# Kernel optimization log

Measured on AMD Instinct MI355X. Metric: run time of the kernel, lower is better.

Reference implementation:

```python
import jax, jax.numpy as jnp
import numpy as np

C = 256
BN_EPS = 1e-5


def conv1x1(x, w, b):
    # x: (B, Cin, H, W), w: (Cout, Cin), b: (Cout,)
    return jnp.einsum('bchw,oc->bohw', x, w) + b[None, :, None, None]


def setup_inputs() -> dict:
    key = jax.random.key(0)
    ks = jax.random.split(key, 12)
    B, H, W = 8, 64, 64
    s = 1.0 / np.sqrt(C)
    inp = {
        'xi': jax.random.normal(ks[0], (B, C, H, W), jnp.float32),
        'xj': jax.random.normal(ks[1], (B, C, H, W), jnp.float32),
        'g_w': jax.random.normal(ks[2], (C, C), jnp.float32) * s,
        'g_b': jax.random.normal(ks[3], (C,), jnp.float32) * s,
        'theta_w': jax.random.normal(ks[4], (C, C), jnp.float32) * s,
        'theta_b': jax.random.normal(ks[5], (C,), jnp.float32) * s,
        'phi_w': jax.random.normal(ks[6], (C, C), jnp.float32) * s,
        'phi_b': jax.random.normal(ks[7], (C,), jnp.float32) * s,
        'W_w': jax.random.normal(ks[8], (C, C), jnp.float32) * s,
        'W_b': jax.random.normal(ks[9], (C,), jnp.float32) * s,
        'bn_gamma': jnp.ones((C,), jnp.float32),
        'bn_beta': jnp.zeros((C,), jnp.float32),
    }
    return inp


def reference(xi, xj, g_w, g_b, theta_w, theta_b, phi_w, phi_b, W_w, W_b, bn_gamma, bn_beta):
    B, Cc, H, W = xi.shape
    N = H * W
    # 1x1 conv projections, flattened to token sequences
    g_x = conv1x1(xj, g_w, g_b).reshape(B, Cc, N)        # (B, C, N)
    theta_x = conv1x1(xi, theta_w, theta_b).reshape(B, Cc, N)  # (B, C, N)
    phi_x = conv1x1(xj, phi_w, phi_b).reshape(B, Cc, N)  # (B, C, N)
    # f = theta^T @ phi, scaled by N (no softmax)
    f = jnp.einsum('bcn,bcm->bnm', theta_x, phi_x) / N   # (B, N, N)
    # y = f @ g^T, back to channel-first
    y = jnp.einsum('bnm,bcm->bcn', f, g_x).reshape(B, Cc, H, W)
    W_y = conv1x1(y, W_w, W_b)
    z = W_y + xi
    # BatchNorm2d (training-mode batch statistics, biased variance)
    mean = jnp.mean(z, axis=(0, 2, 3), keepdims=True)
    var = jnp.var(z, axis=(0, 2, 3), keepdims=True)
    z_hat = (z - mean) * jax.lax.rsqrt(var + BN_EPS)
    return z_hat * bn_gamma[None, :, None, None] + bn_beta[None, :, None, None]
```

## Files before the change

kernel.cpp:

```cpp
#include <hip/hip_runtime.h>
#include <cstddef>

#define CCH 256
#define NPIX 4096
#define NB 8
#define INVCNT (1.0f/32768.0f)
#define INVN (1.0f/4096.0f)

typedef __bf16 bf16_t;
typedef __attribute__((ext_vector_type(8))) __bf16 bf16x8;
typedef __attribute__((ext_vector_type(4))) __bf16 bf16x4;
typedef __attribute__((ext_vector_type(4))) float f32x4;

#define OFF_S      0u
#define OFF_AB     2048u
#define OFF_BMT    34816u
#define OFF_T1     67584u
#define OFF_R      67840u
#define OFF_W1     68096u
#define OFF_C1     68352u
#define OFF_G      68608u
#define OFF_MP     592896u
#define OFF_E      855040u
#define OFF_RSP    857088u
#define OFF_ZPS    889856u
#define OFF_ZPQ    1020928u
#define OFF_SCALE  1152000u
#define OFF_SHIFT  1152256u
#define OFF_GP     1152512u
#define OFF_XIT    7443968u

__device__ __forceinline__ void pack8(const float4& x, const float4& y, bf16x8& o) {
  o[0]=(bf16_t)x.x; o[1]=(bf16_t)x.y; o[2]=(bf16_t)x.z; o[3]=(bf16_t)x.w;
  o[4]=(bf16_t)y.x; o[5]=(bf16_t)y.y; o[6]=(bf16_t)y.z; o[7]=(bf16_t)y.w;
}

__device__ __forceinline__ void ld4(const float* p, float4& a0, float4& a1, float4& a2, float4& a3) {
  a0 = *(const float4*)p;       a1 = *(const float4*)(p + 4);
  a2 = *(const float4*)(p + 8); a3 = *(const float4*)(p + 12);
}

template <bool ATRANS>
__device__ __forceinline__ void mm64_compute(const float* __restrict__ A,
                                             const float* __restrict__ B,
                                             int i0, int j0,
                                             float (&acc)[4][4],
                                             float (*s1)[65], float (*s2)[65]) {
  const int t = threadIdx.x, tx = t & 15, ty = t >> 4;
  for (int k0 = 0; k0 < 256; k0 += 64) {
#pragma unroll
    for (int it = 0; it < 4; ++it) {
      const int f = t + 256 * it;
      const int row = f >> 4, cc = (f & 15) * 4;
      float4 va;
      if (ATRANS)
        va = *(const float4*)(A + (size_t)(k0 + row) * CCH + i0 + cc);
      else
        va = *(const float4*)(A + (size_t)(i0 + row) * CCH + k0 + cc);
      const float4 vb = *(const float4*)(B + (size_t)(k0 + row) * CCH + j0 + cc);
      s1[row][cc + 0] = va.x; s1[row][cc + 1] = va.y; s1[row][cc + 2] = va.z; s1[row][cc + 3] = va.w;
      s2[row][cc + 0] = vb.x; s2[row][cc + 1] = vb.y; s2[row][cc + 2] = vb.z; s2[row][cc + 3] = vb.w;
    }
    __syncthreads();
#pragma unroll 4
    for (int kk = 0; kk < 64; ++kk) {
      float ar[4], br[4];
#pragma unroll
      for (int i = 0; i < 4; ++i) ar[i] = ATRANS ? s1[kk][4 * ty + i] : s1[4 * ty + i][kk];
#pragma unroll
      for (int j = 0; j < 4; ++j) br[j] = s2[kk][4 * tx + j];
#pragma unroll
      for (int i = 0; i < 4; ++i)
#pragma unroll
        for (int j = 0; j < 4; ++j) acc[i][j] += ar[i] * br[j];
    }
    __syncthreads();
  }
}

__device__ void pre_body(int blk, const float* Ww, const float* gw, const float* phw,
                         const float* thw, const float* gb, const float* phb,
                         const float* thb, float* ws, unsigned char* SMEM) {
  const int t = threadIdx.x;
  if (blk < 32) {
    float (*s1)[65] = (float(*)[65])SMEM;
    float (*s2)[65] = (float(*)[65])(SMEM + 16640);
    const int tb = blk & 15;
    const int i0 = (tb >> 2) * 64, j0 = (tb & 3) * 64;
    float acc[4][4] = {};
    if (blk < 16) mm64_compute<false>(Ww, gw, i0, j0, acc, s1, s2);
    else          mm64_compute<true >(thw, phw, i0, j0, acc, s1, s2);
    bf16_t* outp = (bf16_t*)(ws + (blk < 16 ? OFF_AB : OFF_BMT));
    const int tx = t & 15, ty = t >> 4;
#pragma unroll
    for (int i = 0; i < 4; ++i) {
      bf16x4 mv;
#pragma unroll
      for (int q = 0; q < 4; ++q) mv[q] = (bf16_t)acc[i][q];
      *(bf16x4*)&outp[(size_t)(i0 + 4 * ty + i) * CCH + j0 + 4 * tx] = mv;
    }
  } else {
    float t1v = 0.f, rv = 0.f, w1v = 0.f;
    for (int k = 0; k < 256; ++k) {
      t1v += phw[k * CCH + t] * thb[k];
      rv  += thw[k * CCH + t] * phb[k];
      w1v += Ww[t * CCH + k] * gb[k];
    }
    ws[OFF_T1 + t] = t1v; ws[OFF_R + t] = rv; ws[OFF_W1 + t] = w1v;
    float* red = (float*)SMEM;
    red[t] = phb[t] * thb[t];
    __syncthreads();
    for (int off = 128; off; off >>= 1) { if (t < off) red[t] += red[t + off]; __syncthreads(); }
    if (t == 0) ws[OFF_C1] = red[0];
  }
}

__device__ void cvtT_body(int bx, int b, const float* __restrict__ xi,
                          float* __restrict__ ws, unsigned char* SMEM) {
  bf16_t (*st)[72] = (bf16_t(*)[72])SMEM;
  const int c0 = (bx & 3) * 64;
  const int n0 = (bx >> 2) * 64;
  const float* X = xi + (size_t)b * CCH * NPIX;
  const int t = threadIdx.x;
  const int r = t >> 4, c4 = (t & 15) * 4;
#pragma unroll
  for (int it = 0; it < 4; ++it) {
    const int row = r + 16 * it;
    const float4 v = *(const float4*)(X + (size_t)(c0 + row) * NPIX + n0 + c4);
    st[row][c4 + 0] = (bf16_t)v.x; st[row][c4 + 1] = (bf16_t)v.y;
    st[row][c4 + 2] = (bf16_t)v.z; st[row][c4 + 3] = (bf16_t)v.w;
  }
  __syncthreads();
  bf16_t* Xit = (bf16_t*)(ws + OFF_XIT) + (size_t)b * NPIX * CCH;
  const int nr = t >> 2, cc = (t & 3) * 16;
  bf16x8 o0, o1;
#pragma unroll
  for (int j = 0; j < 8; ++j) o0[j] = st[cc + j][nr];
#pragma unroll
  for (int j = 0; j < 8; ++j) o1[j] = st[cc + 8 + j][nr];
  *(bf16x8*)(Xit + (size_t)(n0 + nr) * CCH + c0 + cc) = o0;
  *(bf16x8*)(Xit + (size_t)(n0 + nr) * CCH + c0 + cc + 8) = o1;
}

__device__ void gram_body(int bx, int b, const float* __restrict__ xj,
                          float* __restrict__ ws, unsigned char* SMEM) {
  const int ks = bx & 15;
  const int tl = bx >> 4;
  const int i0 = (tl == 2) ? 128 : 0;
  const int j0 = (tl == 0) ? 0 : 128;
  const float* __restrict__ X = xj + (size_t)b * CCH * NPIX;
  bf16_t (*sA)[128][40] = (bf16_t(*)[128][40])SMEM;
  bf16_t (*sB)[128][40] = (bf16_t(*)[128][40])(SMEM + 20480);
  const int t = threadIdx.x;
  const int w = t >> 6, lane = t & 63;
  const f32x4 z4 = {0.f, 0.f, 0.f, 0.f};
  f32x4 acc[2][8];
#pragma unroll
  for (int fr = 0; fr < 2; ++fr)
#pragma unroll
    for (int fc = 0; fc < 8; ++fc) acc[fr][fc] = z4;
  float rsum = 0.f;
  const int k0 = ks * 256;
  const int srow = t >> 1, sh16 = (t & 1) * 16;
  const bool haveB = (tl == 1);

  float4 a0, a1, a2, a3, b0, b1, b2, b3;
  auto LOAD = [&](int kc) {
    const float* pa = X + (size_t)(i0 + srow) * NPIX + k0 + kc + sh16;
    ld4(pa, a0, a1, a2, a3);
    rsum += a0.x + a0.y + a0.z + a0.w + a1.x + a1.y + a1.z + a1.w
          + a2.x + a2.y + a2.z + a2.w + a3.x + a3.y + a3.z + a3.w;
    if (haveB) {
      const float* pb = X + (size_t)(j0 + srow) * NPIX + k0 + kc + sh16;
      ld4(pb, b0, b1, b2, b3);
    }
  };
  auto WRITE = [&](int q) {
    bf16x8 u0, u1;
    pack8(a0, a1, u0); pack8(a2, a3, u1);
    *(bf16x8*)&sA[q][srow][sh16] = u0;
    *(bf16x8*)&sA[q][srow][sh16 + 8] = u1;
    if (haveB) {
      bf16x8 w0, w1;
      pack8(b0, b1, w0); pack8(b2, b3, w1);
      *(bf16x8*)&sB[q][srow][sh16] = w0;
      *(bf16x8*)&sB[q][srow][sh16 + 8] = w1;
    }
  };

  LOAD(0);
  WRITE(0);
  __syncthreads();
  int cur = 0;
  for (int kc8 = 0; kc8 < 8; ++kc8) {
    if (kc8 < 7) LOAD(32 * (kc8 + 1));
    const int fcol = 8 * (lane >> 4);
    const int lr = lane & 15;
    bf16_t (*SBc)[40] = haveB ? sB[cur] : sA[cur];
    const bf16x8 af0 = *(const bf16x8*)&sA[cur][32 * w + lr][fcol];
    const bf16x8 af1 = *(const bf16x8*)&sA[cur][32 * w + 16 + lr][fcol];
#pragma unroll
    for (int fc = 0; fc < 8; ++fc) {
      const bf16x8 bv = *(const bf16x8*)&SBc[16 * fc + lr][fcol];
      acc[0][fc] = __builtin_amdgcn_mfma_f32_16x16x32_bf16(af0, bv, acc[0][fc], 0, 0, 0);
      acc[1][fc] = __builtin_amdgcn_mfma_f32_16x16x32_bf16(af1, bv, acc[1][fc], 0, 0, 0);
    }
    if (kc8 < 7) WRITE(cur ^ 1);
    __syncthreads();
    cur ^= 1;
  }

  if (tl != 1) {
    const float o = __shfl_down(rsum, 1);
    if (!(t & 1)) ws[OFF_RSP + ((size_t)(b * 16 + ks)) * CCH + i0 + srow] = rsum + o;
  }
  float* GP = ws + OFF_GP + ((size_t)((b * 16 + ks) * 3 + tl)) * 16384;
  const int rbase = 32 * w + ((lane >> 4) << 2);
  const int col = lane & 15;
#pragma unroll
  for (int fr = 0; fr < 2; ++fr)
#pragma unroll
    for (int fc = 0; fc < 8; ++fc)
#pragma unroll
      for (int reg = 0; reg < 4; ++reg)
        GP[(size_t)(rbase + 16 * fr + reg) * 128 + 16 * fc + col] = acc[fr][fc][reg];
}

__global__ __launch_bounds__(256) void k_mega(const float* __restrict__ xi,
                                              const float* __restrict__ xj,
                                              const float* __restrict__ Ww,
                                              const float* __restrict__ gw,
                                              const float* __restrict__ phw,
                                              const float* __restrict__ thw,
                                              const float* __restrict__ gb,
                                              const float* __restrict__ phb,
                                              const float* __restrict__ thb,
                                              float* __restrict__ ws) {
  __shared__ __align__(16) unsigned char SMEM[40960];
  const int bx = blockIdx.x, by = blockIdx.y;
  if (bx >= 304) {
    if (by == 0) pre_body(bx - 304, Ww, gw, phw, thw, gb, phb, thb, ws, SMEM);
    return;
  }
  if (bx >= 48) { cvtT_body(bx - 48, by, xi, ws, SMEM); return; }
  gram_body(bx, by, xj, ws, SMEM);
}

__global__ __launch_bounds__(256) void k_greduce(float* __restrict__ ws) {
  const int b = blockIdx.y, bx = blockIdx.x, t = threadIdx.x;
  const float* BP = ws + OFF_GP + (size_t)b * 48 * 16384;
  float* G = ws + OFF_G + (size_t)b * 65536;
  if (bx < 128) {
    const int i = bx;
    const int j = t;
    const int tl = (j < 128) ? 0 : 1;
    const size_t idx = (size_t)i * 128 + (j & 127);
    float s = 0.f;
#pragma unroll 4
    for (int ks = 0; ks < 16; ++ks) s += BP[((size_t)ks * 3 + tl) * 16384 + idx];
    G[(size_t)i * CCH + j] = s;
    if (j >= 128) G[(size_t)j * CCH + i] = s;
    if (t < 32) {
      const int row = (t < 16) ? i : (i + 128);
      const int l = t & 15;
      float v = ws[OFF_RSP + ((size_t)(b * 16 + l)) * CCH + row];
#pragma unroll
      for (int off = 8; off; off >>= 1) v += __shfl_down(v, off, 16);
      if (l == 0) ws[OFF_S + b * CCH + row] = v;
    }
  } else {
    const int r = 128 + ((bx - 128) << 1) + (t >> 7);
    const int j = 128 + (t & 127);
    const size_t idx = (size_t)(r - 128) * 128 + (j - 128);
    float s = 0.f;
#pragma unroll 4
    for (int ks = 0; ks < 16; ++ks) s += BP[((size_t)ks * 3 + 2) * 16384 + idx];
    G[(size_t)r * CCH + j] = s;
  }
}

__global__ __launch_bounds__(256) void k_kmmat(const float* __restrict__ Wb, float* __restrict__ ws) {
  const int b = blockIdx.y;
  const int i0 = blockIdx.x * 64;
  const int t = threadIdx.x;
  const int w = t >> 6, lane = t & 63;
  const int rg = w >> 1, cg = w & 1;
  const int lr = lane & 15, hi = lane >> 4;
  const int fcol = 8 * hi;

  __shared__ __align__(16) bf16_t sA[2][64][40];
  __shared__ __align__(16) bf16_t sB[2][256][40];
  __shared__ __align__(16) bf16_t sK[64][264];
  __shared__ float sS[256], sT1[256], sR[256], sW1[256], sVS[256];
  __shared__ float sU[64];
  __shared__ float red[256];
  __shared__ float sdt_sh;

  const bf16_t* Ab  = (const bf16_t*)(ws + OFF_AB);
  const bf16_t* BmT = (const bf16_t*)(ws + OFF_BMT);
  const float*  Gf  = ws + OFF_G + (size_t)b * 65536;

  sS[t]  = ws[OFF_S + b * CCH + t];
  sT1[t] = ws[OFF_T1 + t];
  sR[t]  = ws[OFF_R + t];
  sW1[t] = ws[OFF_W1 + t];
  __syncthreads();
  red[t] = sS[t] * sT1[t];
  __syncthreads();
  for (int off = 128; off; off >>= 1) { if (t < off) red[t] += red[t + off]; __syncthreads(); }
  if (t == 0) sdt_sh = red[0];
  {
    float a = 0.f;
    for (int k8 = 0; k8 < 256; k8 += 8) {
      const bf16x8 v = *(const bf16x8*)&BmT[(size_t)t * CCH + k8];
#pragma unroll
      for (int q = 0; q < 8; ++q) a += (float)v[q] * sS[k8 + q];
    }
    sVS[t] = a;
  }
  if (t < 64) {
    float a = 0.f;
    for (int k8 = 0; k8 < 256; k8 += 8) {
      const bf16x8 v = *(const bf16x8*)&Ab[(size_t)(i0 + t) * CCH + k8];
#pragma unroll
      for (int q = 0; q < 8; ++q) a += (float)v[q] * sS[k8 + q];
    }
    sU[t] = a;
  }

  const f32x4 z4 = {0.f, 0.f, 0.f, 0.f};
  const int arow = t >> 2, achk = (t & 3) * 8;

  f32x4 acc[2][8];
#pragma unroll
  for (int fr = 0; fr < 2; ++fr)
#pragma unroll
    for (int fc = 0; fc < 8; ++fc) acc[fr][fc] = z4;
  bf16x8 ra;
  float4 g[4][2];
  auto LOADB = [&](int k) {
    ra = *(const bf16x8*)&Ab[(size_t)(i0 + arow) * CCH + k + achk];
#pragma unroll
    for (int h = 0; h < 4; ++h) {
      const float* p = &Gf[(size_t)(64 * h + arow) * CCH + k + achk];
      g[h][0] = *(const float4*)p;
      g[h][1] = *(const float4*)(p + 4);
    }
  };
  auto WRITEB = [&](int q) {
    *(bf16x8*)&sA[q][arow][achk] = ra;
#pragma unroll
    for (int h = 0; h < 4; ++h) {
      bf16x8 u;
      pack8(g[h][0], g[h][1], u);
      *(bf16x8*)&sB[q][64 * h + arow][achk] = u;
    }
  };
  LOADB(0);
  WRITEB(0);
  __syncthreads();
  int cur = 0;
  for (int ks = 0; ks < 8; ++ks) {
    if (ks < 7) LOADB(32 * (ks + 1));
    const bf16x8 af0 = *(const bf16x8*)&sA[cur][32 * rg + lr][fcol];
    const bf16x8 af1 = *(const bf16x8*)&sA[cur][32 * rg + 16 + lr][fcol];
#pragma unroll
    for (int fc = 0; fc < 8; ++fc) {
      const bf16x8 bv = *(const bf16x8*)&sB[cur][128 * cg + 16 * fc + lr][fcol];
      acc[0][fc] = __builtin_amdgcn_mfma_f32_16x16x32_bf16(af0, bv, acc[0][fc], 0, 0, 0);
      acc[1][fc] = __builtin_amdgcn_mfma_f32_16x16x32_bf16(af1, bv, acc[1][fc], 0, 0, 0);
    }
    if (ks < 7) WRITEB(cur ^ 1);
    __syncthreads();
    cur ^= 1;
  }
#pragma unroll
  for (int fr = 0; fr < 2; ++fr)
#pragma unroll
    for (int fc = 0; fc < 8; ++fc)
#pragma unroll
      for (int reg = 0; reg < 4; ++reg)
        sK[32 * rg + 16 * fr + 4 * hi + reg][128 * cg + 16 * fc + lr] = (bf16_t)acc[fr][fc][reg];
  __syncthreads();

  if (t < 64) {
    float dot = 0.f;
    for (int k8 = 0; k8 < 256; k8 += 8) {
      const bf16x8 v = *(const bf16x8*)&sK[t][k8];
#pragma unroll
      for (int q = 0; q < 8; ++q) dot += (float)v[q] * sT1[k8 + q];
    }
    const float c1 = ws[OFF_C1];
    const float ui = sU[t], w1i = sW1[i0 + t];
    ws[OFF_E + b * CCH + i0 + t] = INVN * (dot + c1 * ui + sdt_sh * w1i) + c1 * w1i + Wb[i0 + t];
  }

  f32x4 acc2[2][8];
#pragma unroll
  for (int fr = 0; fr < 2; ++fr)
#pragma unroll
    for (int fc = 0; fc < 8; ++fc) acc2[fr][fc] = z4;
  bf16x8 rb[4];
  auto LOADC = [&](int k) {
#pragma unroll
    for (int h = 0; h < 4; ++h)
      rb[h] = *(const bf16x8*)&BmT[(size_t)(64 * h + arow) * CCH + k + achk];
  };
  auto WRITEC = [&](int q) {
#pragma unroll
    for (int h = 0; h < 4; ++h)
      *(bf16x8*)&sB[q][64 * h + arow][achk] = rb[h];
  };
  LOADC(0);
  WRITEC(0);
  __syncthreads();
  cur = 0;
  for (int ks = 0; ks < 8; ++ks) {
    if (ks < 7) LOADC(32 * (ks + 1));
    const bf16x8 af0 = *(const bf16x8*)&sK[32 * rg + lr][32 * ks + fcol];
    const bf16x8 af1 = *(const bf16x8*)&sK[32 * rg + 16 + lr][32 * ks + fcol];
#pragma unroll
    for (int fc = 0; fc < 8; ++fc) {
      const bf16x8 bv = *(const bf16x8*)&sB[cur][128 * cg + 16 * fc + lr][fcol];
      acc2[0][fc] = __builtin_amdgcn_mfma_f32_16x16x32_bf16(af0, bv, acc2[0][fc], 0, 0, 0);
      acc2[1][fc] = __builtin_amdgcn_mfma_f32_16x16x32_bf16(af1, bv, acc2[1][fc], 0, 0, 0);
    }
    if (ks < 7) WRITEC(cur ^ 1);
    __syncthreads();
    cur ^= 1;
  }

  bf16_t* Mp = (bf16_t*)(ws + OFF_MP) + (size_t)b * 65536;
#pragma unroll
  for (int fr = 0; fr < 2; ++fr)
#pragma unroll
    for (int fc = 0; fc < 8; ++fc) {
      const int j = 128 * cg + 16 * fc + lr;
      const float rj = sR[j], vsj = sVS[j];
#pragma unroll
      for (int reg = 0; reg < 4; ++reg) {
        const int il = 32 * rg + 16 * fr + 4 * hi + reg;
        const float ui = sU[il], w1i = sW1[i0 + il];
        float m = (acc2[fr][fc][reg] + ui * rj + w1i * vsj) * INVN + w1i * rj;
        if (i0 + il == j) m += 1.0f;
        Mp[(size_t)(i0 + il) * CCH + j] = (bf16_t)m;
      }
    }
}

template <int APPLY>
__global__ __launch_bounds__(256) void k_zmm(float* __restrict__ ws, float* __restrict__ out) {
  const int b = blockIdx.y, nblk = blockIdx.x;
  const int n0 = nblk * 64;
  const int t = threadIdx.x;
  const int w = t >> 6, lane = t & 63;
  const int rg = w >> 1, cg = w & 1;
  __shared__ __align__(16) bf16_t sA[2][64][40];
  __shared__ __align__(16) bf16_t sB[2][256][40];
  __shared__ float sC1[256], sC2[256];
  __shared__ float redS[4][128], redQ[4][128];
  {
    const float e = ws[OFF_E + b * CCH + t];
    if (APPLY) {
      const float sc = ws[OFF_SCALE + t];
      sC1[t] = sc;
      sC2[t] = e * sc + ws[OFF_SHIFT + t];
    } else {
      sC1[t] = e;
    }
  }
  const bf16_t* Xit = (const bf16_t*)(ws + OFF_XIT) + (size_t)b * NPIX * CCH;
  const bf16_t* Mp = (const bf16_t*)(ws + OFF_MP) + (size_t)b * 65536;
  const f32x4 z4 = {0.f, 0.f, 0.f, 0.f};
  f32x4 acc[2][8];
#pragma unroll
  for (int fr = 0; fr < 2; ++fr)
#pragma unroll
    for (int fc = 0; fc < 8; ++fc) acc[fr][fc] = z4;
  const int arow = t >> 2, achk = (t & 3) * 8;
  bf16x8 ra, rb0, rb1, rb2, rb3;
  ra  = *(const bf16x8*)(Xit + (size_t)(n0 + arow) * CCH + achk);
  rb0 = *(const bf16x8*)(Mp + (size_t)(arow)       * CCH + achk);
  rb1 = *(const bf16x8*)(Mp + (size_t)(64 + arow)  * CCH + achk);
  rb2 = *(const bf16x8*)(Mp + (size_t)(128 + arow) * CCH + achk);
  rb3 = *(const bf16x8*)(Mp + (size_t)(192 + arow) * CCH + achk);
  *(bf16x8*)&sA[0][arow][achk] = ra;
  *(bf16x8*)&sB[0][arow][achk] = rb0;
  *(bf16x8*)&sB[0][64 + arow][achk] = rb1;
  *(bf16x8*)&sB[0][128 + arow][achk] = rb2;
  *(bf16x8*)&sB[0][192 + arow][achk] = rb3;
  __syncthreads();
  int cur = 0;
  for (int ks = 0; ks < 8; ++ks) {
    const int nk = 32 * (ks + 1);
    if (ks < 7) {
      ra  = *(const bf16x8*)(Xit + (size_t)(n0 + arow) * CCH + nk + achk);
      rb0 = *(const bf16x8*)(Mp + (size_t)(arow)       * CCH + nk + achk);
      rb1 = *(const bf16x8*)(Mp + (size_t)(64 + arow)  * CCH + nk + achk);
      rb2 = *(const bf16x8*)(Mp + (size_t)(128 + arow) * CCH + nk + achk);
      rb3 = *(const bf16x8*)(Mp + (size_t)(192 + arow) * CCH + nk + achk);
    }
    const int fcol = 8 * (lane >> 4);
    const int lr = lane & 15;
    const bf16x8 af0 = *(const bf16x8*)&sA[cur][32 * rg + lr][fcol];
    const bf16x8 af1 = *(const bf16x8*)&sA[cur][32 * rg + 16 + lr][fcol];
#pragma unroll
    for (int fc = 0; fc < 8; ++fc) {
      const bf16x8 bv = *(const bf16x8*)&sB[cur][128 * cg + 16 * fc + lr][fcol];
      acc[0][fc] = __builtin_amdgcn_mfma_f32_16x16x32_bf16(af0, bv, acc[0][fc], 0, 0, 0);
      acc[1][fc] = __builtin_amdgcn_mfma_f32_16x16x32_bf16(af1, bv, acc[1][fc], 0, 0, 0);
    }
    if (ks < 7) {
      *(bf16x8*)&sA[cur ^ 1][arow][achk] = ra;
      *(bf16x8*)&sB[cur ^ 1][arow][achk] = rb0;
      *(bf16x8*)&sB[cur ^ 1][64 + arow][achk] = rb1;
      *(bf16x8*)&sB[cur ^ 1][128 + arow][achk] = rb2;
      *(bf16x8*)&sB[cur ^ 1][192 + arow][achk] = rb3;
    }
    __syncthreads();
    cur ^= 1;
  }
  if (APPLY) {
#pragma unroll
    for (int fc = 0; fc < 8; ++fc) {
      const int c = 128 * cg + 16 * fc + (lane & 15);
      const float sc = sC1[c], b2 = sC2[c];
      float* op = out + ((size_t)b * CCH + c) * NPIX + n0 + 32 * rg + ((lane >> 4) << 2);
#pragma unroll
      for (int fr = 0; fr < 2; ++fr) {
        float4 v;
        v.x = acc[fr][fc][0] * sc + b2;
        v.y = acc[fr][fc][1] * sc + b2;
        v.z = acc[fr][fc][2] * sc + b2;
        v.w = acc[fr][fc][3] * sc + b2;
        *(float4*)(op + 16 * fr) = v;
      }
    }
  } else {
    float ps[8], pq[8];
#pragma unroll
    for (int fc = 0; fc < 8; ++fc) {
      const int c = 128 * cg + 16 * fc + (lane & 15);
      const float e = sC1[c];
      float s = 0.f, q = 0.f;
#pragma unroll
      for (int fr = 0; fr < 2; ++fr)
#pragma unroll
        for (int reg = 0; reg < 4; ++reg) {
          const float z = acc[fr][fc][reg] + e;
          s += z; q += z * z;
        }
      s += __shfl_xor(s, 16); s += __shfl_xor(s, 32);
      q += __shfl_xor(q, 16); q += __shfl_xor(q, 32);
      ps[fc] = s; pq[fc] = q;
    }
    if (lane < 16) {
#pragma unroll
      for (int fc = 0; fc < 8; ++fc) {
        redS[w][16 * fc + lane] = ps[fc];
        redQ[w][16 * fc + lane] = pq[fc];
      }
    }
    __syncthreads();
    if (t < 256) {
      const int cg2 = t >> 7, c = t & 127;
      float s = 0.f, q = 0.f;
#pragma unroll
      for (int rg2 = 0; rg2 < 2; ++rg2) {
        s += redS[rg2 * 2 + cg2][c];
        q += redQ[rg2 * 2 + cg2][c];
      }
      ws[OFF_ZPS + (size_t)t * 512 + b * 64 + nblk] = s;
      ws[OFF_ZPQ + (size_t)t * 512 + b * 64 + nblk] = q;
    }
  }
}

__global__ __launch_bounds__(64) void k_bnstats(const float* __restrict__ gamma,
                                                const float* __restrict__ beta,
                                                float* __restrict__ ws) {
  const int c = blockIdx.x, t = threadIdx.x;
  const float* PS = ws + OFF_ZPS + (size_t)c * 512;
  const float* PQ = ws + OFF_ZPQ + (size_t)c * 512;
  float s = 0.f, q = 0.f;
#pragma unroll
  for (int e = 0; e < 8; ++e) { s += PS[t + 64 * e]; q += PQ[t + 64 * e]; }
#pragma unroll
  for (int off = 32; off; off >>= 1) { s += __shfl_down(s, off); q += __shfl_down(q, off); }
  if (t == 0) {
    const float mean = s * INVCNT;
    const float var = q * INVCNT - mean * mean;
    const float sc = gamma[c] * rsqrtf(var + 1e-5f);
    ws[OFF_SCALE + c] = sc;
    ws[OFF_SHIFT + c] = beta[c] - mean * sc;
  }
}

extern "C" void kernel_launch(void* const* d_in, const int* in_sizes, int n_in,
                              void* d_out, int out_size, void* d_ws, size_t ws_size,
                              hipStream_t stream) {
  const float* xi  = (const float*)d_in[0];
  const float* xj  = (const float*)d_in[1];
  const float* gw  = (const float*)d_in[2];
  const float* gb  = (const float*)d_in[3];
  const float* thw = (const float*)d_in[4];
  const float* thb = (const float*)d_in[5];
  const float* phw = (const float*)d_in[6];
  const float* phb = (const float*)d_in[7];
  const float* Ww  = (const float*)d_in[8];
  const float* Wb  = (const float*)d_in[9];
  const float* gamma = (const float*)d_in[10];
  const float* beta  = (const float*)d_in[11];
  float* ws = (float*)d_ws;
  float* out = (float*)d_out;

  k_mega<<<dim3(337, 8), 256, 0, stream>>>(xi, xj, Ww, gw, phw, thw, gb, phb, thb, ws);
  k_greduce<<<dim3(192, 8), 256, 0, stream>>>(ws);
  k_kmmat<<<dim3(4, 8), 256, 0, stream>>>(Wb, ws);
  k_zmm<0><<<dim3(64, 8), 256, 0, stream>>>(ws, out);
  k_bnstats<<<256, 64, 0, stream>>>(gamma, beta, ws);
  k_zmm<1><<<dim3(64, 8), 256, 0, stream>>>(ws, out);
}
```

Measured before the change: 98.83 us.

## Cut Gram split-K partials, store Gram in bf16, stage output stores via LDS

The Gram-matrix split-K factor drops from 16 to 4 slices per batch, so each block runs a longer K loop. This shrinks the partial-sum buffer and the reduction traffic, at the cost of fewer parallel blocks. The reduced Gram matrix is now written as bf16, which halves its storage and removes the float-to-bf16 packing in the consumer kernel, with extra rounding before the MFMA. The final normalized-output write is transposed through shared memory so each thread emits contiguous float4 runs along pixels, adding two barriers per half.

Result: slower. 108.2 us (+9.4%).

```diff
diff --git a/kernel.cpp b/kernel.cpp
--- a/kernel.cpp
+++ b/kernel.cpp
@@ -20,15 +20,15 @@
 #define OFF_W1     68096u
 #define OFF_C1     68352u
 #define OFF_G      68608u
-#define OFF_MP     592896u
-#define OFF_E      855040u
-#define OFF_RSP    857088u
-#define OFF_ZPS    889856u
-#define OFF_ZPQ    1020928u
-#define OFF_SCALE  1152000u
-#define OFF_SHIFT  1152256u
-#define OFF_GP     1152512u
-#define OFF_XIT    7443968u
+#define OFF_MP     330752u
+#define OFF_E      592896u
+#define OFF_RSP    594944u
+#define OFF_ZPS    603136u
+#define OFF_ZPQ    734208u
+#define OFF_SCALE  865280u
+#define OFF_SHIFT  865536u
+#define OFF_GP     865792u
+#define OFF_XIT    2438656u
 
 __device__ __forceinline__ void pack8(const float4& x, const float4& y, bf16x8& o) {
   o[0]=(bf16_t)x.x; o[1]=(bf16_t)x.y; o[2]=(bf16_t)x.z; o[3]=(bf16_t)x.w;
@@ -144,8 +144,8 @@
 
 __device__ void gram_body(int bx, int b, const float* __restrict__ xj,
                           float* __restrict__ ws, unsigned char* SMEM) {
-  const int ks = bx & 15;
-  const int tl = bx >> 4;
+  const int ks = bx & 3;
+  const int tl = bx >> 2;
   const int i0 = (tl == 2) ? 128 : 0;
   const int j0 = (tl == 0) ? 0 : 128;
   const float* __restrict__ X = xj + (size_t)b * CCH * NPIX;
@@ -160,7 +160,7 @@
 #pragma unroll
     for (int fc = 0; fc < 8; ++fc) acc[fr][fc] = z4;
   float rsum = 0.f;
-  const int k0 = ks * 256;
+  const int k0 = ks * 1024;
   const int srow = t >> 1, sh16 = (t & 1) * 16;
   const bool haveB = (tl == 1);
 
@@ -192,8 +192,8 @@
   WRITE(0);
   __syncthreads();
   int cur = 0;
-  for (int kc8 = 0; kc8 < 8; ++kc8) {
-    if (kc8 < 7) LOAD(32 * (kc8 + 1));
+  for (int kc8 = 0; kc8 < 32; ++kc8) {
+    if (kc8 < 31) LOAD(32 * (kc8 + 1));
     const int fcol = 8 * (lane >> 4);
     const int lr = lane & 15;
     bf16_t (*SBc)[40] = haveB ? sB[cur] : sA[cur];
@@ -205,16 +205,16 @@
       acc[0][fc] = __builtin_amdgcn_mfma_f32_16x16x32_bf16(af0, bv, acc[0][fc], 0, 0, 0);
       acc[1][fc] = __builtin_amdgcn_mfma_f32_16x16x32_bf16(af1, bv, acc[1][fc], 0, 0, 0);
     }
-    if (kc8 < 7) WRITE(cur ^ 1);
+    if (kc8 < 31) WRITE(cur ^ 1);
     __syncthreads();
     cur ^= 1;
   }
 
   if (tl != 1) {
     const float o = __shfl_down(rsum, 1);
-    if (!(t & 1)) ws[OFF_RSP + ((size_t)(b * 16 + ks)) * CCH + i0 + srow] = rsum + o;
-  }
-  float* GP = ws + OFF_GP + ((size_t)((b * 16 + ks) * 3 + tl)) * 16384;
+    if (!(t & 1)) ws[OFF_RSP + ((size_t)(b * 4 + ks)) * CCH + i0 + srow] = rsum + o;
+  }
+  float* GP = ws + OFF_GP + ((size_t)((b * 4 + ks) * 3 + tl)) * 16384;
   const int rbase = 32 * w + ((lane >> 4) << 2);
   const int col = lane & 15;
 #pragma unroll
@@ -238,32 +238,32 @@
                                               float* __restrict__ ws) {
   __shared__ __align__(16) unsigned char SMEM[40960];
   const int bx = blockIdx.x, by = blockIdx.y;
-  if (bx >= 304) {
-    if (by == 0) pre_body(bx - 304, Ww, gw, phw, thw, gb, phb, thb, ws, SMEM);
+  if (bx >= 268) {
+    if (by == 0) pre_body(bx - 268, Ww, gw, phw, thw, gb, phb, thb, ws, SMEM);
     return;
   }
-  if (bx >= 48) { cvtT_body(bx - 48, by, xi, ws, SMEM); return; }
+  if (bx >= 12) { cvtT_body(bx - 12, by, xi, ws, SMEM); return; }
   gram_body(bx, by, xj, ws, SMEM);
 }
 
 __global__ __launch_bounds__(256) void k_greduce(float* __restrict__ ws) {
   const int b = blockIdx.y, bx = blockIdx.x, t = threadIdx.x;
-  const float* BP = ws + OFF_GP + (size_t)b * 48 * 16384;
-  float* G = ws + OFF_G + (size_t)b * 65536;
+  const float* BP = ws + OFF_GP + (size_t)b * 12 * 16384;
+  bf16_t* Gb = (bf16_t*)(ws + OFF_G) + (size_t)b * 65536;
   if (bx < 128) {
     const int i = bx;
     const int j = t;
     const int tl = (j < 128) ? 0 : 1;
     const size_t idx = (size_t)i * 128 + (j & 127);
     float s = 0.f;
-#pragma unroll 4
-    for (int ks = 0; ks < 16; ++ks) s += BP[((size_t)ks * 3 + tl) * 16384 + idx];
-    G[(size_t)i * CCH + j] = s;
-    if (j >= 128) G[(size_t)j * CCH + i] = s;
+#pragma unroll
+    for (int ks = 0; ks < 4; ++ks) s += BP[((size_t)ks * 3 + tl) * 16384 + idx];
+    Gb[(size_t)i * CCH + j] = (bf16_t)s;
+    if (j >= 128) Gb[(size_t)j * CCH + i] = (bf16_t)s;
     if (t < 32) {
       const int row = (t < 16) ? i : (i + 128);
       const int l = t & 15;
-      float v = ws[OFF_RSP + ((size_t)(b * 16 + l)) * CCH + row];
+      float v = (l < 4) ? ws[OFF_RSP + ((size_t)(b * 4 + l)) * CCH + row] : 0.f;
 #pragma unroll
       for (int off = 8; off; off >>= 1) v += __shfl_down(v, off, 16);
       if (l == 0) ws[OFF_S + b * CCH + row] = v;
@@ -273,9 +273,9 @@
     const int j = 128 + (t & 127);
     const size_t idx = (size_t)(r - 128) * 128 + (j - 128);
     float s = 0.f;
-#pragma unroll 4
-    for (int ks = 0; ks < 16; ++ks) s += BP[((size_t)ks * 3 + 2) * 16384 + idx];
-    G[(size_t)r * CCH + j] = s;
+#pragma unroll
+    for (int ks = 0; ks < 4; ++ks) s += BP[((size_t)ks * 3 + 2) * 16384 + idx];
+    Gb[(size_t)r * CCH + j] = (bf16_t)s;
   }
 }
 
@@ -298,7 +298,7 @@
 
   const bf16_t* Ab  = (const bf16_t*)(ws + OFF_AB);
   const bf16_t* BmT = (const bf16_t*)(ws + OFF_BMT);
-  const float*  Gf  = ws + OFF_G + (size_t)b * 65536;
+  const bf16_t* Gb  = (const bf16_t*)(ws + OFF_G) + (size_t)b * 65536;
 
   sS[t]  = ws[OFF_S + b * CCH + t];
   sT1[t] = ws[OFF_T1 + t];
@@ -337,24 +337,18 @@
 #pragma unroll
     for (int fc = 0; fc < 8; ++fc) acc[fr][fc] = z4;
   bf16x8 ra;
-  float4 g[4][2];
+  bf16x8 gb8[4];
   auto LOADB = [&](int k) {
     ra = *(const bf16x8*)&Ab[(size_t)(i0 + arow) * CCH + k + achk];
 #pragma unroll
-    for (int h = 0; h < 4; ++h) {
-      const float* p = &Gf[(size_t)(64 * h + arow) * CCH + k + achk];
-      g[h][0] = *(const float4*)p;
-      g[h][1] = *(const float4*)(p + 4);
-    }
+    for (int h = 0; h < 4; ++h)
+      gb8[h] = *(const bf16x8*)&Gb[(size_t)(64 * h + arow) * CCH + k + achk];
   };
   auto WRITEB = [&](int q) {
     *(bf16x8*)&sA[q][arow][achk] = ra;
 #pragma unroll
-    for (int h = 0; h < 4; ++h) {
-      bf16x8 u;
-      pack8(g[h][0], g[h][1], u);
-      *(bf16x8*)&sB[q][64 * h + arow][achk] = u;
-    }
+    for (int h = 0; h < 4; ++h)
+      *(bf16x8*)&sB[q][64 * h + arow][achk] = gb8[h];
   };
   LOADB(0);
   WRITEB(0);
@@ -455,8 +449,10 @@
   const int t = threadIdx.x;
   const int w = t >> 6, lane = t & 63;
   const int rg = w >> 1, cg = w & 1;
-  __shared__ __align__(16) bf16_t sA[2][64][40];
-  __shared__ __align__(16) bf16_t sB[2][256][40];
+  __shared__ __align__(16) unsigned char SMEMu[51200];
+  bf16_t (*sA)[64][40]  = (bf16_t(*)[64][40])SMEMu;
+  bf16_t (*sB)[256][40] = (bf16_t(*)[256][40])(SMEMu + 10240);
+  float (*sZ)[68]       = (float(*)[68])SMEMu;
   __shared__ float sC1[256], sC2[256];
   __shared__ float redS[4][128], redQ[4][128];
   {
@@ -521,19 +517,31 @@
     cur ^= 1;
   }
   if (APPLY) {
-#pragma unroll
-    for (int fc = 0; fc < 8; ++fc) {
-      const int c = 128 * cg + 16 * fc + (lane & 15);
+    const int lr = lane & 15, hi = lane >> 4;
+    for (int h = 0; h < 2; ++h) {
+      __syncthreads();
+      if (cg == h) {
+#pragma unroll
+        for (int fr = 0; fr < 2; ++fr)
+#pragma unroll
+          for (int fc = 0; fc < 8; ++fc)
+#pragma unroll
+            for (int reg = 0; reg < 4; ++reg)
+              sZ[16 * fc + lr][32 * rg + 16 * fr + 4 * hi + reg] = acc[fr][fc][reg];
+      }
+      __syncthreads();
+      const int rr = t >> 1, nq = (t & 1) * 32;
+      const int c = 128 * h + rr;
       const float sc = sC1[c], b2 = sC2[c];
-      float* op = out + ((size_t)b * CCH + c) * NPIX + n0 + 32 * rg + ((lane >> 4) << 2);
-#pragma unroll
-      for (int fr = 0; fr < 2; ++fr) {
+      float* op = out + ((size_t)b * CCH + c) * NPIX + n0 + nq;
+#pragma unroll
+      for (int q = 0; q < 8; ++q) {
         float4 v;
-        v.x = acc[fr][fc][0] * sc + b2;
-        v.y = acc[fr][fc][1] * sc + b2;
-        v.z = acc[fr][fc][2] * sc + b2;
-        v.w = acc[fr][fc][3] * sc + b2;
-        *(float4*)(op + 16 * fr) = v;
+        v.x = sZ[rr][nq + 4 * q + 0] * sc + b2;
+        v.y = sZ[rr][nq + 4 * q + 1] * sc + b2;
+        v.z = sZ[rr][nq + 4 * q + 2] * sc + b2;
+        v.w = sZ[rr][nq + 4 * q + 3] * sc + b2;
+        *(float4*)(op + 4 * q) = v;
       }
     }
   } else {
@@ -614,7 +622,7 @@
   float* ws = (float*)d_ws;
   float* out = (float*)d_out;
 
-  k_mega<<<dim3(337, 8), 256, 0, stream>>>(xi, xj, Ww, gw, phw, thw, gb, phb, thb, ws);
+  k_mega<<<dim3(301, 8), 256, 0, stream>>>(xi, xj, Ww, gw, phw, thw, gb, phb, thb, ws);
   k_greduce<<<dim3(192, 8), 256, 0, stream>>>(ws);
   k_kmmat<<<dim3(4, 8), 256, 0, stream>>>(Wb, ws);
   k_zmm<0><<<dim3(64, 8), 256, 0, stream>>>(ws, out);
```

## Compute full Gram tile per block with 512 threads and store partials in bf16

Applied to the files above, without the earlier changes.

The Gram stage now has each 512-thread block compute the full 256x256 Gram partial for its K slice from one shared tile, instead of three symmetric 128x128 tiles that reloaded xj rows. Partials and the reduced G matrix are stored as bf16, which halves traffic through greduce and kmmat and lets kmmat skip the fp32-to-bf16 packing. The pre and transpose bodies are re-tiled for 512 threads, and kmmat uses 32-row tiles to double its grid. In exchange, G is now summed and stored in bf16, which loses precision, and the larger blocks with more accumulators raise register pressure.

New measurement: 87.46 us. -11.5%, faster.

```diff
diff --git a/kernel.cpp b/kernel.cpp
--- a/kernel.cpp
+++ b/kernel.cpp
@@ -20,15 +20,15 @@
 #define OFF_W1     68096u
 #define OFF_C1     68352u
 #define OFF_G      68608u
-#define OFF_MP     592896u
-#define OFF_E      855040u
-#define OFF_RSP    857088u
-#define OFF_ZPS    889856u
-#define OFF_ZPQ    1020928u
-#define OFF_SCALE  1152000u
-#define OFF_SHIFT  1152256u
-#define OFF_GP     1152512u
-#define OFF_XIT    7443968u
+#define OFF_MP     330752u
+#define OFF_E      592896u
+#define OFF_RSP    594944u
+#define OFF_ZPS    627712u
+#define OFF_ZPQ    758784u
+#define OFF_SCALE  889856u
+#define OFF_SHIFT  890112u
+#define OFF_GP     890368u
+#define OFF_XIT    5084672u
 
 __device__ __forceinline__ void pack8(const float4& x, const float4& y, bf16x8& o) {
   o[0]=(bf16_t)x.x; o[1]=(bf16_t)x.y; o[2]=(bf16_t)x.z; o[3]=(bf16_t)x.w;
@@ -41,16 +41,16 @@
 }
 
 template <bool ATRANS>
-__device__ __forceinline__ void mm64_compute(const float* __restrict__ A,
-                                             const float* __restrict__ B,
-                                             int i0, int j0,
-                                             float (&acc)[4][4],
-                                             float (*s1)[65], float (*s2)[65]) {
+__device__ __forceinline__ void mm64v(const float* __restrict__ A,
+                                      const float* __restrict__ B,
+                                      int i0, int j0,
+                                      float (&acc)[2][4],
+                                      float (*s1)[65], float (*s2)[65]) {
   const int t = threadIdx.x, tx = t & 15, ty = t >> 4;
   for (int k0 = 0; k0 < 256; k0 += 64) {
 #pragma unroll
-    for (int it = 0; it < 4; ++it) {
-      const int f = t + 256 * it;
+    for (int it = 0; it < 2; ++it) {
+      const int f = t + 512 * it;
       const int row = f >> 4, cc = (f & 15) * 4;
       float4 va;
       if (ATRANS)
@@ -64,13 +64,13 @@
     __syncthreads();
 #pragma unroll 4
     for (int kk = 0; kk < 64; ++kk) {
-      float ar[4], br[4];
-#pragma unroll
-      for (int i = 0; i < 4; ++i) ar[i] = ATRANS ? s1[kk][4 * ty + i] : s1[4 * ty + i][kk];
+      float ar[2], br[4];
+#pragma unroll
+      for (int i = 0; i < 2; ++i) ar[i] = ATRANS ? s1[kk][2 * ty + i] : s1[2 * ty + i][kk];
 #pragma unroll
       for (int j = 0; j < 4; ++j) br[j] = s2[kk][4 * tx + j];
 #pragma unroll
-      for (int i = 0; i < 4; ++i)
+      for (int i = 0; i < 2; ++i)
 #pragma unroll
         for (int j = 0; j < 4; ++j) acc[i][j] += ar[i] * br[j];
     }
@@ -87,30 +87,32 @@
     float (*s2)[65] = (float(*)[65])(SMEM + 16640);
     const int tb = blk & 15;
     const int i0 = (tb >> 2) * 64, j0 = (tb & 3) * 64;
-    float acc[4][4] = {};
-    if (blk < 16) mm64_compute<false>(Ww, gw, i0, j0, acc, s1, s2);
-    else          mm64_compute<true >(thw, phw, i0, j0, acc, s1, s2);
+    float acc[2][4] = {};
+    if (blk < 16) mm64v<false>(Ww, gw, i0, j0, acc, s1, s2);
+    else          mm64v<true >(thw, phw, i0, j0, acc, s1, s2);
     bf16_t* outp = (bf16_t*)(ws + (blk < 16 ? OFF_AB : OFF_BMT));
     const int tx = t & 15, ty = t >> 4;
 #pragma unroll
-    for (int i = 0; i < 4; ++i) {
+    for (int i = 0; i < 2; ++i) {
       bf16x4 mv;
 #pragma unroll
       for (int q = 0; q < 4; ++q) mv[q] = (bf16_t)acc[i][q];
-      *(bf16x4*)&outp[(size_t)(i0 + 4 * ty + i) * CCH + j0 + 4 * tx] = mv;
+      *(bf16x4*)&outp[(size_t)(i0 + 2 * ty + i) * CCH + j0 + 4 * tx] = mv;
     }
   } else {
-    float t1v = 0.f, rv = 0.f, w1v = 0.f;
-    for (int k = 0; k < 256; ++k) {
-      t1v += phw[k * CCH + t] * thb[k];
-      rv  += thw[k * CCH + t] * phb[k];
-      w1v += Ww[t * CCH + k] * gb[k];
-    }
-    ws[OFF_T1 + t] = t1v; ws[OFF_R + t] = rv; ws[OFF_W1 + t] = w1v;
+    if (t < 256) {
+      float t1v = 0.f, rv = 0.f, w1v = 0.f;
+      for (int k = 0; k < 256; ++k) {
+        t1v += phw[k * CCH + t] * thb[k];
+        rv  += thw[k * CCH + t] * phb[k];
+        w1v += Ww[t * CCH + k] * gb[k];
+      }
+      ws[OFF_T1 + t] = t1v; ws[OFF_R + t] = rv; ws[OFF_W1 + t] = w1v;
+    }
     float* red = (float*)SMEM;
-    red[t] = phb[t] * thb[t];
-    __syncthreads();
-    for (int off = 128; off; off >>= 1) { if (t < off) red[t] += red[t + off]; __syncthreads(); }
+    red[t] = (t < 256) ? phb[t] * thb[t] : 0.f;
+    __syncthreads();
+    for (int off = 256; off; off >>= 1) { if (t < off) red[t] += red[t + off]; __syncthreads(); }
     if (t == 0) ws[OFF_C1] = red[0];
   }
 }
@@ -118,21 +120,22 @@
 __device__ void cvtT_body(int bx, int b, const float* __restrict__ xi,
                           float* __restrict__ ws, unsigned char* SMEM) {
   bf16_t (*st)[72] = (bf16_t(*)[72])SMEM;
-  const int c0 = (bx & 3) * 64;
-  const int n0 = (bx >> 2) * 64;
+  const int c0 = (bx & 1) * 128;
+  const int n0 = (bx >> 1) * 64;
   const float* X = xi + (size_t)b * CCH * NPIX;
   const int t = threadIdx.x;
-  const int r = t >> 4, c4 = (t & 15) * 4;
-#pragma unroll
-  for (int it = 0; it < 4; ++it) {
-    const int row = r + 16 * it;
-    const float4 v = *(const float4*)(X + (size_t)(c0 + row) * NPIX + n0 + c4);
-    st[row][c4 + 0] = (bf16_t)v.x; st[row][c4 + 1] = (bf16_t)v.y;
-    st[row][c4 + 2] = (bf16_t)v.z; st[row][c4 + 3] = (bf16_t)v.w;
+  const int r = t >> 2, c4 = (t & 3) * 16;
+  {
+    float4 a0, a1, a2, a3;
+    ld4(X + (size_t)(c0 + r) * NPIX + n0 + c4, a0, a1, a2, a3);
+    bf16x8 u0, u1;
+    pack8(a0, a1, u0); pack8(a2, a3, u1);
+    *(bf16x8*)&st[r][c4] = u0;
+    *(bf16x8*)&st[r][c4 + 8] = u1;
   }
   __syncthreads();
   bf16_t* Xit = (bf16_t*)(ws + OFF_XIT) + (size_t)b * NPIX * CCH;
-  const int nr = t >> 2, cc = (t & 3) * 16;
+  const int nr = t >> 3, cc = (t & 7) * 16;
   bf16x8 o0, o1;
 #pragma unroll
   for (int j = 0; j < 8; ++j) o0[j] = st[cc + j][nr];
@@ -142,50 +145,36 @@
   *(bf16x8*)(Xit + (size_t)(n0 + nr) * CCH + c0 + cc + 8) = o1;
 }
 
-__device__ void gram_body(int bx, int b, const float* __restrict__ xj,
+__device__ void gram_body(int ks, int b, const float* __restrict__ xj,
                           float* __restrict__ ws, unsigned char* SMEM) {
-  const int ks = bx & 15;
-  const int tl = bx >> 4;
-  const int i0 = (tl == 2) ? 128 : 0;
-  const int j0 = (tl == 0) ? 0 : 128;
   const float* __restrict__ X = xj + (size_t)b * CCH * NPIX;
-  bf16_t (*sA)[128][40] = (bf16_t(*)[128][40])SMEM;
-  bf16_t (*sB)[128][40] = (bf16_t(*)[128][40])(SMEM + 20480);
+  bf16_t (*sA)[256][40] = (bf16_t(*)[256][40])SMEM;
   const int t = threadIdx.x;
   const int w = t >> 6, lane = t & 63;
+  const int wr = w >> 1, wc = w & 1;
+  const int lr = lane & 15, hi = lane >> 4;
+  const int fcol = 8 * hi;
   const f32x4 z4 = {0.f, 0.f, 0.f, 0.f};
-  f32x4 acc[2][8];
-#pragma unroll
-  for (int fr = 0; fr < 2; ++fr)
+  f32x4 acc[4][8];
+#pragma unroll
+  for (int fr = 0; fr < 4; ++fr)
 #pragma unroll
     for (int fc = 0; fc < 8; ++fc) acc[fr][fc] = z4;
   float rsum = 0.f;
   const int k0 = ks * 256;
   const int srow = t >> 1, sh16 = (t & 1) * 16;
-  const bool haveB = (tl == 1);
-
-  float4 a0, a1, a2, a3, b0, b1, b2, b3;
+
+  float4 a0, a1, a2, a3;
   auto LOAD = [&](int kc) {
-    const float* pa = X + (size_t)(i0 + srow) * NPIX + k0 + kc + sh16;
-    ld4(pa, a0, a1, a2, a3);
+    ld4(X + (size_t)srow * NPIX + k0 + kc + sh16, a0, a1, a2, a3);
     rsum += a0.x + a0.y + a0.z + a0.w + a1.x + a1.y + a1.z + a1.w
           + a2.x + a2.y + a2.z + a2.w + a3.x + a3.y + a3.z + a3.w;
-    if (haveB) {
-      const float* pb = X + (size_t)(j0 + srow) * NPIX + k0 + kc + sh16;
-      ld4(pb, b0, b1, b2, b3);
-    }
   };
   auto WRITE = [&](int q) {
     bf16x8 u0, u1;
     pack8(a0, a1, u0); pack8(a2, a3, u1);
     *(bf16x8*)&sA[q][srow][sh16] = u0;
     *(bf16x8*)&sA[q][srow][sh16 + 8] = u1;
-    if (haveB) {
-      bf16x8 w0, w1;
-      pack8(b0, b1, w0); pack8(b2, b3, w1);
-      *(bf16x8*)&sB[q][srow][sh16] = w0;
-      *(bf16x8*)&sB[q][srow][sh16 + 8] = w1;
-    }
   };
 
   LOAD(0);
@@ -194,39 +183,38 @@
   int cur = 0;
   for (int kc8 = 0; kc8 < 8; ++kc8) {
     if (kc8 < 7) LOAD(32 * (kc8 + 1));
-    const int fcol = 8 * (lane >> 4);
-    const int lr = lane & 15;
-    bf16_t (*SBc)[40] = haveB ? sB[cur] : sA[cur];
-    const bf16x8 af0 = *(const bf16x8*)&sA[cur][32 * w + lr][fcol];
-    const bf16x8 af1 = *(const bf16x8*)&sA[cur][32 * w + 16 + lr][fcol];
+    bf16x8 af[4];
+#pragma unroll
+    for (int fr = 0; fr < 4; ++fr)
+      af[fr] = *(const bf16x8*)&sA[cur][64 * wr + 16 * fr + lr][fcol];
 #pragma unroll
     for (int fc = 0; fc < 8; ++fc) {
-      const bf16x8 bv = *(const bf16x8*)&SBc[16 * fc + lr][fcol];
-      acc[0][fc] = __builtin_amdgcn_mfma_f32_16x16x32_bf16(af0, bv, acc[0][fc], 0, 0, 0);
-      acc[1][fc] = __builtin_amdgcn_mfma_f32_16x16x32_bf16(af1, bv, acc[1][fc], 0, 0, 0);
+      const bf16x8 bv = *(const bf16x8*)&sA[cur][128 * wc + 16 * fc + lr][fcol];
+#pragma unroll
+      for (int fr = 0; fr < 4; ++fr)
+        acc[fr][fc] = __builtin_amdgcn_mfma_f32_16x16x32_bf16(af[fr], bv, acc[fr][fc], 0, 0, 0);
     }
     if (kc8 < 7) WRITE(cur ^ 1);
     __syncthreads();
     cur ^= 1;
   }
 
-  if (tl != 1) {
+  {
     const float o = __shfl_down(rsum, 1);
-    if (!(t & 1)) ws[OFF_RSP + ((size_t)(b * 16 + ks)) * CCH + i0 + srow] = rsum + o;
-  }
-  float* GP = ws + OFF_GP + ((size_t)((b * 16 + ks) * 3 + tl)) * 16384;
-  const int rbase = 32 * w + ((lane >> 4) << 2);
-  const int col = lane & 15;
-#pragma unroll
-  for (int fr = 0; fr < 2; ++fr)
+    if (!(t & 1)) ws[OFF_RSP + ((size_t)(b * 16 + ks)) * CCH + srow] = rsum + o;
+  }
+  bf16_t* GPp = (bf16_t*)(ws + OFF_GP) + (size_t)(b * 16 + ks) * 65536;
+#pragma unroll
+  for (int fr = 0; fr < 4; ++fr)
 #pragma unroll
     for (int fc = 0; fc < 8; ++fc)
 #pragma unroll
       for (int reg = 0; reg < 4; ++reg)
-        GP[(size_t)(rbase + 16 * fr + reg) * 128 + 16 * fc + col] = acc[fr][fc][reg];
-}
-
-__global__ __launch_bounds__(256) void k_mega(const float* __restrict__ xi,
+        GPp[(size_t)(64 * wr + 16 * fr + 4 * hi + reg) * CCH + 128 * wc + 16 * fc + lr] =
+            (bf16_t)acc[fr][fc][reg];
+}
+
+__global__ __launch_bounds__(512) void k_mega(const float* __restrict__ xi,
                                               const float* __restrict__ xj,
                                               const float* __restrict__ Ww,
                                               const float* __restrict__ gw,
@@ -238,67 +226,60 @@
                                               float* __restrict__ ws) {
   __shared__ __align__(16) unsigned char SMEM[40960];
   const int bx = blockIdx.x, by = blockIdx.y;
-  if (bx >= 304) {
-    if (by == 0) pre_body(bx - 304, Ww, gw, phw, thw, gb, phb, thb, ws, SMEM);
+  if (bx >= 144) {
+    if (by == 0) pre_body(bx - 144, Ww, gw, phw, thw, gb, phb, thb, ws, SMEM);
     return;
   }
-  if (bx >= 48) { cvtT_body(bx - 48, by, xi, ws, SMEM); return; }
+  if (bx >= 16) { cvtT_body(bx - 16, by, xi, ws, SMEM); return; }
   gram_body(bx, by, xj, ws, SMEM);
 }
 
 __global__ __launch_bounds__(256) void k_greduce(float* __restrict__ ws) {
   const int b = blockIdx.y, bx = blockIdx.x, t = threadIdx.x;
-  const float* BP = ws + OFF_GP + (size_t)b * 48 * 16384;
-  float* G = ws + OFF_G + (size_t)b * 65536;
-  if (bx < 128) {
-    const int i = bx;
-    const int j = t;
-    const int tl = (j < 128) ? 0 : 1;
-    const size_t idx = (size_t)i * 128 + (j & 127);
-    float s = 0.f;
-#pragma unroll 4
-    for (int ks = 0; ks < 16; ++ks) s += BP[((size_t)ks * 3 + tl) * 16384 + idx];
-    G[(size_t)i * CCH + j] = s;
-    if (j >= 128) G[(size_t)j * CCH + i] = s;
-    if (t < 32) {
-      const int row = (t < 16) ? i : (i + 128);
-      const int l = t & 15;
-      float v = ws[OFF_RSP + ((size_t)(b * 16 + l)) * CCH + row];
-#pragma unroll
-      for (int off = 8; off; off >>= 1) v += __shfl_down(v, off, 16);
-      if (l == 0) ws[OFF_S + b * CCH + row] = v;
-    }
-  } else {
-    const int r = 128 + ((bx - 128) << 1) + (t >> 7);
-    const int j = 128 + (t & 127);
-    const size_t idx = (size_t)(r - 128) * 128 + (j - 128);
-    float s = 0.f;
-#pragma unroll 4
-    for (int ks = 0; ks < 16; ++ks) s += BP[((size_t)ks * 3 + 2) * 16384 + idx];
-    G[(size_t)r * CCH + j] = s;
+  const bf16_t* GPp = (const bf16_t*)(ws + OFF_GP) + (size_t)b * 16 * 65536;
+  bf16_t* Gb = (bf16_t*)(ws + OFF_G) + (size_t)b * 65536;
+  const int row = bx * 8 + (t >> 5);
+  const int j8 = (t & 31) * 8;
+  float s[8] = {};
+#pragma unroll
+  for (int ks = 0; ks < 16; ++ks) {
+    const bf16x8 v = *(const bf16x8*)&GPp[(size_t)ks * 65536 + row * CCH + j8];
+#pragma unroll
+    for (int q = 0; q < 8; ++q) s[q] += (float)v[q];
+  }
+  bf16x8 o;
+#pragma unroll
+  for (int q = 0; q < 8; ++q) o[q] = (bf16_t)s[q];
+  *(bf16x8*)&Gb[(size_t)row * CCH + j8] = o;
+  if (t < 128) {
+    const int rr = bx * 8 + (t >> 4), l = t & 15;
+    float v = ws[OFF_RSP + ((size_t)(b * 16 + l)) * CCH + rr];
+#pragma unroll
+    for (int off = 8; off; off >>= 1) v += __shfl_down(v, off, 16);
+    if (l == 0) ws[OFF_S + b * CCH + rr] = v;
   }
 }
 
 __global__ __launch_bounds__(256) void k_kmmat(const float* __restrict__ Wb, float* __restrict__ ws) {
   const int b = blockIdx.y;
-  const int i0 = blockIdx.x * 64;
+  const int i0 = blockIdx.x * 32;
   const int t = threadIdx.x;
   const int w = t >> 6, lane = t & 63;
   const int rg = w >> 1, cg = w & 1;
   const int lr = lane & 15, hi = lane >> 4;
   const int fcol = 8 * hi;
 
-  __shared__ __align__(16) bf16_t sA[2][64][40];
+  __shared__ __align__(16) bf16_t sA[2][32][40];
   __shared__ __align__(16) bf16_t sB[2][256][40];
-  __shared__ __align__(16) bf16_t sK[64][264];
+  __shared__ __align__(16) bf16_t sK[32][264];
   __shared__ float sS[256], sT1[256], sR[256], sW1[256], sVS[256];
-  __shared__ float sU[64];
+  __shared__ float sU[32];
   __shared__ float red[256];
   __shared__ float sdt_sh;
 
   const bf16_t* Ab  = (const bf16_t*)(ws + OFF_AB);
   const bf16_t* BmT = (const bf16_t*)(ws + OFF_BMT);
-  const float*  Gf  = ws + OFF_G + (size_t)b * 65536;
+  const bf16_t* Gb  = (const bf16_t*)(ws + OFF_G) + (size_t)b * 65536;
 
   sS[t]  = ws[OFF_S + b * CCH + t];
   sT1[t] = ws[OFF_T1 + t];
@@ -318,7 +299,7 @@
     }
     sVS[t] = a;
   }
-  if (t < 64) {
+  if (t < 32) {
     float a = 0.f;
     for (int k8 = 0; k8 < 256; k8 += 8) {
       const bf16x8 v = *(const bf16x8*)&Ab[(size_t)(i0 + t) * CCH + k8];
@@ -330,31 +311,24 @@
 
   const f32x4 z4 = {0.f, 0.f, 0.f, 0.f};
   const int arow = t >> 2, achk = (t & 3) * 8;
-
-  f32x4 acc[2][8];
-#pragma unroll
-  for (int fr = 0; fr < 2; ++fr)
-#pragma unroll
-    for (int fc = 0; fc < 8; ++fc) acc[fr][fc] = z4;
+  const int arA = t >> 2, akA = (t & 3) * 8;
+
+  f32x4 acc[8];
+#pragma unroll
+  for (int fc = 0; fc < 8; ++fc) acc[fc] = z4;
   bf16x8 ra;
-  float4 g[4][2];
+  bf16x8 gb8[4];
   auto LOADB = [&](int k) {
-    ra = *(const bf16x8*)&Ab[(size_t)(i0 + arow) * CCH + k + achk];
-#pragma unroll
-    for (int h = 0; h < 4; ++h) {
-      const float* p = &Gf[(size_t)(64 * h + arow) * CCH + k + achk];
-      g[h][0] = *(const float4*)p;
-      g[h][1] = *(const float4*)(p + 4);
-    }
+    if (t < 128) ra = *(const bf16x8*)&Ab[(size_t)(i0 + arA) * CCH + k + akA];
+#pragma unroll
+    for (int h = 0; h < 4; ++h)
+      gb8[h] = *(const bf16x8*)&Gb[(size_t)(64 * h + arow) * CCH + k + achk];
   };
   auto WRITEB = [&](int q) {
-    *(bf16x8*)&sA[q][arow][achk] = ra;
-#pragma unroll
-    for (int h = 0; h < 4; ++h) {
-      bf16x8 u;
-      pack8(g[h][0], g[h][1], u);
-      *(bf16x8*)&sB[q][64 * h + arow][achk] = u;
-    }
+    if (t < 128) *(bf16x8*)&sA[q][arA][akA] = ra;
+#pragma unroll
+    for (int h = 0; h < 4; ++h)
+      *(bf16x8*)&sB[q][64 * h + arow][achk] = gb8[h];
   };
   LOADB(0);
   WRITEB(0);
@@ -362,28 +336,24 @@
   int cur = 0;
   for (int ks = 0; ks < 8; ++ks) {
     if (ks < 7) LOADB(32 * (ks + 1));
-    const bf16x8 af0 = *(const bf16x8*)&sA[cur][32 * rg + lr][fcol];
-    const bf16x8 af1 = *(const bf16x8*)&sA[cur][32 * rg + 16 + lr][fcol];
+    const bf16x8 af = *(const bf16x8*)&sA[cur][16 * rg + lr][fcol];
 #pragma unroll
     for (int fc = 0; fc < 8; ++fc) {
       const bf16x8 bv = *(const bf16x8*)&sB[cur][128 * cg + 16 * fc + lr][fcol];
-      acc[0][fc] = __builtin_amdgcn_mfma_f32_16x16x32_bf16(af0, bv, acc[0][fc], 0, 0, 0);
-      acc[1][fc] = __builtin_amdgcn_mfma_f32_16x16x32_bf16(af1, bv, acc[1][fc], 0, 0, 0);
+      acc[fc] = __builtin_amdgcn_mfma_f32_16x16x32_bf16(af, bv, acc[fc], 0, 0, 0);
     }
     if (ks < 7) WRITEB(cur ^ 1);
     __syncthreads();
     cur ^= 1;
   }
 #pragma unroll
-  for (int fr = 0; fr < 2; ++fr)
-#pragma unroll
-    for (int fc = 0; fc < 8; ++fc)
-#pragma unroll
-      for (int reg = 0; reg < 4; ++reg)
-        sK[32 * rg + 16 * fr + 4 * hi + reg][128 * cg + 16 * fc + lr] = (bf16_t)acc[fr][fc][reg];
-  __syncthreads();
-
-  if (t < 64) {
+  for (int fc = 0; fc < 8; ++fc)
+#pragma unroll
+    for (int reg = 0; reg < 4; ++reg)
+      sK[16 * rg + 4 * hi + reg][128 * cg + 16 * fc + lr] = (bf16_t)acc[fc][reg];
+  __syncthreads();
+
+  if (t < 32) {
     float dot = 0.f;
     for (int k8 = 0; k8 < 256; k8 += 8) {
       const bf16x8 v = *(const bf16x8*)&sK[t][k8];
@@ -395,11 +365,9 @@
     ws[OFF_E + b * CCH + i0 + t] = INVN * (dot + c1 * ui + sdt_sh * w1i) + c1 * w1i + Wb[i0 + t];
   }
 
-  f32x4 acc2[2][8];
-#pragma unroll
-  for (int fr = 0; fr < 2; ++fr)
-#pragma unroll
-    for (int fc = 0; fc < 8; ++fc) acc2[fr][fc] = z4;
+  f32x4 acc2[8];
+#pragma unroll
+  for (int fc = 0; fc < 8; ++fc) acc2[fc] = z4;
   bf16x8 rb[4];
   auto LOADC = [&](int k) {
 #pragma unroll
@@ -417,13 +385,11 @@
   cur = 0;
   for (int ks = 0; ks < 8; ++ks) {
     if (ks < 7) LOADC(32 * (ks + 1));
-    const bf16x8 af0 = *(const bf16x8*)&sK[32 * rg + lr][32 * ks + fcol];
-    const bf16x8 af1 = *(const bf16x8*)&sK[32 * rg + 16 + lr][32 * ks + fcol];
+    const bf16x8 af = *(const bf16x8*)&sK[16 * rg + lr][32 * ks + fcol];
 #pragma unroll
     for (int fc = 0; fc < 8; ++fc) {
       const bf16x8 bv = *(const bf16x8*)&sB[cur][128 * cg + 16 * fc + lr][fcol];
-      acc2[0][fc] = __builtin_amdgcn_mfma_f32_16x16x32_bf16(af0, bv, acc2[0][fc], 0, 0, 0);
-      acc2[1][fc] = __builtin_amdgcn_mfma_f32_16x16x32_bf16(af1, bv, acc2[1][fc], 0, 0, 0);
+      acc2[fc] = __builtin_amdgcn_mfma_f32_16x16x32_bf16(af, bv, acc2[fc], 0, 0, 0);
     }
     if (ks < 7) WRITEC(cur ^ 1);
     __syncthreads();
@@ -432,20 +398,18 @@
 
   bf16_t* Mp = (bf16_t*)(ws + OFF_MP) + (size_t)b * 65536;
 #pragma unroll
-  for (int fr = 0; fr < 2; ++fr)
-#pragma unroll
-    for (int fc = 0; fc < 8; ++fc) {
-      const int j = 128 * cg + 16 * fc + lr;
-      const float rj = sR[j], vsj = sVS[j];
-#pragma unroll
-      for (int reg = 0; reg < 4; ++reg) {
-        const int il = 32 * rg + 16 * fr + 4 * hi + reg;
-        const float ui = sU[il], w1i = sW1[i0 + il];
-        float m = (acc2[fr][fc][reg] + ui * rj + w1i * vsj) * INVN + w1i * rj;
-        if (i0 + il == j) m += 1.0f;
-        Mp[(size_t)(i0 + il) * CCH + j] = (bf16_t)m;
-      }
-    }
+  for (int fc = 0; fc < 8; ++fc) {
+    const int j = 128 * cg + 16 * fc + lr;
+    const float rj = sR[j], vsj = sVS[j];
+#pragma unroll
+    for (int reg = 0; reg < 4; ++reg) {
+      const int il = 16 * rg + 4 * hi + reg;
+      const float ui = sU[il], w1i = sW1[i0 + il];
+      float m = (acc2[fc][reg] + ui * rj + w1i * vsj) * INVN + w1i * rj;
+      if (i0 + il == j) m += 1.0f;
+      Mp[(size_t)(i0 + il) * CCH + j] = (bf16_t)m;
+    }
+  }
 }
 
 template <int APPLY>
@@ -614,9 +578,9 @@
   float* ws = (float*)d_ws;
   float* out = (float*)d_out;
 
-  k_mega<<<dim3(337, 8), 256, 0, stream>>>(xi, xj, Ww, gw, phw, thw, gb, phb, thb, ws);
-  k_greduce<<<dim3(192, 8), 256, 0, stream>>>(ws);
-  k_kmmat<<<dim3(4, 8), 256, 0, stream>>>(Wb, ws);
+  k_mega<<<dim3(177, 8), 512, 0, stream>>>(xi, xj, Ww, gw, phw, thw, gb, phb, thb, ws);
+  k_greduce<<<dim3(32, 8), 256, 0, stream>>>(ws);
+  k_kmmat<<<dim3(8, 8), 256, 0, stream>>>(Wb, ws);
   k_zmm<0><<<dim3(64, 8), 256, 0, stream>>>(ws, out);
   k_bnstats<<<256, 64, 0, stream>>>(gamma, beta, ws);
   k_zmm<1><<<dim3(64, 8), 256, 0, stream>>>(ws, out);
```
